# Kernel tuning notes

Measured on AMD Instinct MI355X. Metric: run time of the kernel, lower is better.

## Reference

```python
import jax, jax.numpy as jnp
import numpy as np

N = 100000
E = 640000
IN_DIM = 128
HID = 128
NUM_REL = 8


def _rgcn_layer(x, rel_w, root_w, bias, src, dst, edge_type, num_nodes):
    # PyG RGCNConv: out = x @ root + bias + sum_r mean_{edges of rel r into v}(x_src) @ W_r
    out = x @ root_w + bias
    x_src = x[src]  # [E, d_in]
    for r in range(NUM_REL):
        w = (edge_type == r).astype(x.dtype)  # [E]
        msg_sum = jax.ops.segment_sum(x_src * w[:, None], dst, num_segments=num_nodes)
        cnt = jax.ops.segment_sum(w, dst, num_segments=num_nodes)
        agg = msg_sum / jnp.maximum(cnt, 1.0)[:, None]  # mean aggregation per relation
        out = out + agg @ rel_w[r]
    return out


def setup_inputs() -> dict:
    key = jax.random.key(0)
    ks = jax.random.split(key, 10)
    x = jax.random.normal(ks[0], (N, IN_DIM), dtype=jnp.float32)
    edge_index = jax.random.randint(ks[1], (2, E), 0, N, dtype=jnp.int64)
    edge_type = jax.random.randint(ks[2], (E,), 0, NUM_REL, dtype=jnp.int64)
    s1 = 1.0 / np.sqrt(IN_DIM)
    s2 = 1.0 / np.sqrt(HID)
    rel_w1 = jax.random.uniform(ks[3], (NUM_REL, IN_DIM, HID), jnp.float32, -s1, s1)
    root_w1 = jax.random.uniform(ks[4], (IN_DIM, HID), jnp.float32, -s1, s1)
    b1 = jnp.zeros((HID,), jnp.float32)
    rel_w2 = jax.random.uniform(ks[5], (NUM_REL, HID, HID), jnp.float32, -s2, s2)
    root_w2 = jax.random.uniform(ks[6], (HID, HID), jnp.float32, -s2, s2)
    b2 = jnp.zeros((HID,), jnp.float32)
    return {"x": x, "edge_index": edge_index, "edge_type": edge_type,
            "rel_w1": rel_w1, "root_w1": root_w1, "b1": b1,
            "rel_w2": rel_w2, "root_w2": root_w2, "b2": b2}


def reference(x, edge_index, edge_type, rel_w1, root_w1, b1, rel_w2, root_w2, b2):
    src, dst = edge_index[0], edge_index[1]
    h = _rgcn_layer(x, rel_w1, root_w1, b1, src, dst, edge_type, N)
    h = jax.nn.relu(h)  # dropout p=0.0 -> identity
    h = _rgcn_layer(h, rel_w2, root_w2, b2, src, dst, edge_type, N)
    h = jax.nn.relu(h)
    return h
```

## Files before the change

kernel.cpp:

```cpp
#include <hip/hip_runtime.h>
#include <hip/hip_bf16.h>

#define NN 100000
#define EE 640000
#define DD 128
#define RR 8
#define K8 (NN * RR)
#define NSB2 196
#define GBMAX 11571

typedef __attribute__((ext_vector_type(8))) short short8;
typedef __attribute__((ext_vector_type(4))) float floatx4;
typedef __attribute__((ext_vector_type(4))) unsigned int uint4v;

__device__ __forceinline__ unsigned short f2bf(float f) {
  unsigned int u = __float_as_uint(f);
  u += 0x7FFFu + ((u >> 16) & 1u);
  return (unsigned short)(u >> 16);
}
__device__ __forceinline__ unsigned int pk2bf(float a, float b) {
  __hip_bfloat162 h = __float22bfloat162_rn(make_float2(a, b));
  unsigned int u;
  __builtin_memcpy(&u, &h, 4);
  return u;
}
__device__ __forceinline__ float bflo(unsigned int u) { return __uint_as_float(u << 16); }
__device__ __forceinline__ float bfhi(unsigned int u) { return __uint_as_float(u & 0xFFFF0000u); }

__global__ __launch_bounds__(256) void xb_prep(
    const float* __restrict__ x, unsigned int* __restrict__ xb)
{
  int g = blockIdx.x * 256 + threadIdx.x;
  int v = g >> 4, seg = g & 15;
  const float4* s4 = (const float4*)(x + (size_t)v * 128 + seg * 8);
  float4 a = s4[0], b = s4[1];
  uint4v o;
  o[0] = pk2bf(a.x, a.y); o[1] = pk2bf(a.z, a.w);
  o[2] = pk2bf(b.x, b.y); o[3] = pk2bf(b.z, b.w);
  *(uint4v*)(xb + (size_t)v * 64 + seg * 4) = o;
}

__global__ __launch_bounds__(256) void w_prep_all(
    const float* __restrict__ rel1, const float* __restrict__ root1,
    const float* __restrict__ rel2, const float* __restrict__ root2,
    unsigned short* __restrict__ wt)
{
  int id = blockIdx.x * 256 + threadIdx.x;
  int set = id >= 147456;
  int rem = id - set * 147456;
  int r = rem >> 14, n = (rem >> 7) & 127, k = rem & 127;
  const float* rel = set ? rel2 : rel1;
  const float* root = set ? root2 : root1;
  float v = (r < RR) ? rel[((size_t)r * DD + k) * DD + n] : root[(size_t)k * DD + n];
  wt[id] = f2bf(v);
}

__global__ __launch_bounds__(256) void count_all(
    const int* __restrict__ ei, const int* __restrict__ et,
    int* __restrict__ cntdr, unsigned char* __restrict__ used,
    int* __restrict__ erank)
{
  int e = blockIdx.x * 256 + threadIdx.x;
  int src = ei[e], dst = ei[EE + e], r = et[e];
  erank[e] = atomicAdd(&cntdr[dst * RR + r], 1);
  used[r * NN + src] = 1;
}

__global__ __launch_bounds__(256) void scan_a(
    const int4* __restrict__ c4, int n4, int* __restrict__ bsum)
{
  int t = threadIdx.x;
  int s = 0;
#pragma unroll
  for (int i = 0; i < 4; ++i) {
    int idx = blockIdx.x * 1024 + i * 256 + t;
    if (idx < n4) { int4 v = c4[idx]; s += v.x + v.y + v.z + v.w; }
  }
  __shared__ int wsum[4];
  for (int d = 32; d; d >>= 1) s += __shfl_xor(s, d, 64);
  if ((t & 63) == 0) wsum[t >> 6] = s;
  __syncthreads();
  if (t == 0) bsum[blockIdx.x] = wsum[0] + wsum[1] + wsum[2] + wsum[3];
}

__global__ __launch_bounds__(256) void scan_a_u8(
    const uint4v* __restrict__ c, int n16, int* __restrict__ bsum)
{
  int t = threadIdx.x;
  int idx = blockIdx.x * 256 + t;
  int s = 0;
  if (idx < n16) {
    uint4v v = c[idx];
#pragma unroll
    for (int w = 0; w < 4; ++w) {
      unsigned u = v[w];
      s += ((u & 0x000000FFu) ? 1 : 0) + ((u & 0x0000FF00u) ? 1 : 0)
         + ((u & 0x00FF0000u) ? 1 : 0) + ((u & 0xFF000000u) ? 1 : 0);
    }
  }
  __shared__ int wsum[4];
  for (int d = 32; d; d >>= 1) s += __shfl_xor(s, d, 64);
  if ((t & 63) == 0) wsum[t >> 6] = s;
  __syncthreads();
  if (t == 0) bsum[blockIdx.x] = wsum[0] + wsum[1] + wsum[2] + wsum[3];
}

__global__ void scan_b(const int* __restrict__ bsum, int nsb,
                       int* __restrict__ bbase, int* __restrict__ tot)
{
  int lane = threadIdx.x;
  int v[4]; int s = 0;
#pragma unroll
  for (int i = 0; i < 4; ++i) {
    int idx = lane * 4 + i;
    v[i] = (idx < nsb) ? bsum[idx] : 0; s += v[i];
  }
  int inc = s;
  for (int d = 1; d < 64; d <<= 1) {
    int o = __shfl_up(inc, d, 64);
    if (lane >= d) inc += o;
  }
  int running = inc - s;
#pragma unroll
  for (int i = 0; i < 4; ++i) {
    int idx = lane * 4 + i;
    if (idx < nsb) { bbase[idx] = running; running += v[i]; }
  }
  if (lane == 63 && tot != nullptr) tot[0] = inc;
}

__global__ __launch_bounds__(256) void scan_c(
    const int* __restrict__ cnt, const int* __restrict__ bbase, int n,
    int* __restrict__ out0)
{
  int t = threadIdx.x;
  int base = blockIdx.x * 4096 + t * 16;
  int v[16]; int s = 0;
#pragma unroll
  for (int i = 0; i < 16; ++i) {
    int idx = base + i;
    v[i] = (idx < n) ? cnt[idx] : 0;
    s += v[i];
  }
  int lane = t & 63, wid = t >> 6;
  int inc = s;
  for (int d = 1; d < 64; d <<= 1) {
    int o = __shfl_up(inc, d, 64);
    if (lane >= d) inc += o;
  }
  __shared__ int wsum[4];
  if (lane == 63) wsum[wid] = inc;
  __syncthreads();
  int wb = 0;
  for (int w = 0; w < wid; ++w) wb += wsum[w];
  int running = bbase[blockIdx.x] + wb + (inc - s);
#pragma unroll
  for (int i = 0; i < 16; ++i) {
    int idx = base + i;
    if (idx < n) { out0[idx] = running; running += v[i]; }
  }
  if (blockIdx.x == 0 && t == 0) out0[n] = EE;
}

__global__ __launch_bounds__(256) void scan_c_u8(
    const unsigned char* __restrict__ used, const int* __restrict__ bbase, int n,
    int* __restrict__ out0, int* __restrict__ ubp)
{
  int t = threadIdx.x;
  int base = blockIdx.x * 4096 + t * 16;
  int v[16]; int s = 0;
  if (base < n) {
    uint4v u = *(const uint4v*)(used + base);
    unsigned um[4]; *(uint4v*)um = u;
#pragma unroll
    for (int w = 0; w < 4; ++w)
#pragma unroll
      for (int b = 0; b < 4; ++b) {
        v[w * 4 + b] = ((um[w] >> (8 * b)) & 0xFFu) != 0;
        s += v[w * 4 + b];
      }
  } else {
#pragma unroll
    for (int i = 0; i < 16; ++i) v[i] = 0;
  }
  int lane = t & 63, wid = t >> 6;
  int inc = s;
  for (int d = 1; d < 64; d <<= 1) {
    int o = __shfl_up(inc, d, 64);
    if (lane >= d) inc += o;
  }
  __shared__ int wsum[4];
  if (lane == 63) wsum[wid] = inc;
  __syncthreads();
  int wb = 0;
  for (int w = 0; w < wid; ++w) wb += wsum[w];
  int running = bbase[blockIdx.x] + wb + (inc - s);
#pragma unroll
  for (int i = 0; i < 16; ++i) {
    int idx = base + i;
    if (idx < n) {
      if (idx % NN == 0) ubp[idx / NN] = running;
      out0[idx] = v[i] ? running : -1;
      running += v[i];
    }
  }
}

__global__ void pb_kernel(const int* __restrict__ ub, const int* __restrict__ tot,
                          int* __restrict__ pb)
{
  if (threadIdx.x == 0) {
    int base = 0;
    for (int r = 0; r < RR; ++r) {
      pb[r] = base;
      int hi = (r == RR - 1) ? tot[0] : ub[r + 1];
      int u = hi - ub[r];
      base += (u + 63) & ~63;
    }
    pb[8] = base;
    pb[9] = base + ((NN + 63) & ~63);
  }
}

__global__ __launch_bounds__(256) void fix_kernel(
    int* __restrict__ pidx, const int* __restrict__ ub,
    const int* __restrict__ pb, int* __restrict__ ysrc)
{
  int key = blockIdx.x * 256 + threadIdx.x;
  int g = pidx[key];
  if (g < 0) return;
  int r = key / NN, src = key - r * NN;
  int y = pb[r] + (g - ub[r]);
  pidx[key] = y;
  ysrc[y] = src;
}

__global__ __launch_bounds__(256) void place2(
    const int* __restrict__ ei, const int* __restrict__ et,
    const int* __restrict__ rowptr_dr, const int* __restrict__ pidx,
    const int* __restrict__ erank, int2* __restrict__ recs)
{
  int e = blockIdx.x * 256 + threadIdx.x;
  int src = ei[e], dst = ei[EE + e], r = et[e];
  int k = dst * RR + r;
  int b0 = rowptr_dr[k], b1 = rowptr_dr[k + 1];
  int slot = b0 + erank[e];
  float s = 1.0f / (float)max(b1 - b0, 1);
  int2 rec; rec.x = pidx[r * NN + src]; rec.y = __float_as_int(s);
  recs[slot] = rec;
}

__global__ __launch_bounds__(256, 3) void gemm_y(
    const unsigned int* __restrict__ Xb,
    const unsigned short* __restrict__ Wt,
    const int* __restrict__ ysrc,
    const int* __restrict__ pb,
    unsigned int* __restrict__ Ypk)
{
  const int yrow0 = blockIdx.x * 64;
  if (yrow0 >= pb[9]) return;
  int r = 8;
#pragma unroll
  for (int rr = 0; rr < 8; ++rr) if (yrow0 < pb[rr + 1]) { r = rr; break; }

  __shared__ unsigned short As[64 * 128];
  const int tid = threadIdx.x;
  const int wave = tid >> 6, lane = tid & 63;
  const int quad = lane >> 4, mr = lane & 15;
  const int pb8 = pb[8];

  {
    int row = tid >> 2, q = tid & 3;
    int yrow = yrow0 + row;
    int src;
    if (r < RR) src = ysrc[yrow];
    else { src = yrow - pb8; if (src >= NN) src = 0; }
    const uint4v* xs = (const uint4v*)(Xb + (size_t)src * 64 + q * 16);
#pragma unroll
    for (int c = 0; c < 4; ++c) {
      uint4v v = xs[c];
      int pos = (q * 32 + c * 8 + (row & 15) * 8) & 127;
      *(uint4v*)&As[row * 128 + pos] = v;
    }
  }
  const unsigned short* wr = Wt + (size_t)r * 16384 + (size_t)(wave * 32 + mr) * 128 + quad * 8;
  short8 b0[4], b1[4];
#pragma unroll
  for (int ks = 0; ks < 4; ++ks) {
    b0[ks] = *(const short8*)(wr + ks * 32);
    b1[ks] = *(const short8*)(wr + 16 * 128 + ks * 32);
  }
  __syncthreads();

  floatx4 acc[4][2];
#pragma unroll
  for (int mi = 0; mi < 4; ++mi) {
    acc[mi][0] = (floatx4){0.f, 0.f, 0.f, 0.f};
    acc[mi][1] = (floatx4){0.f, 0.f, 0.f, 0.f};
  }
#pragma unroll
  for (int ks = 0; ks < 4; ++ks) {
    short8 a[4];
#pragma unroll
    for (int mi = 0; mi < 4; ++mi)
      a[mi] = *(const short8*)&As[(mi * 16 + mr) * 128 +
                                  ((ks * 32 + quad * 8 + mr * 8) & 127)];
#pragma unroll
    for (int mi = 0; mi < 4; ++mi) {
      acc[mi][0] = __builtin_amdgcn_mfma_f32_16x16x32_bf16(a[mi], b0[ks], acc[mi][0], 0, 0, 0);
      acc[mi][1] = __builtin_amdgcn_mfma_f32_16x16x32_bf16(a[mi], b1[ks], acc[mi][1], 0, 0, 0);
    }
  }
#pragma unroll
  for (int mi = 0; mi < 4; ++mi)
#pragma unroll
    for (int rg = 0; rg < 4; ++rg)
      Ypk[(size_t)(yrow0 + mi * 16 + quad * 4 + rg) * 64 + wave * 16 + mr] =
          pk2bf(acc[mi][0][rg], acc[mi][1][rg]);
}

__global__ __launch_bounds__(256) void aggregate(
    const unsigned int* __restrict__ Ypk,
    const int* __restrict__ rowptr,
    const int2* __restrict__ recs,
    const int* __restrict__ pb,
    const float* __restrict__ bias,
    void* __restrict__ outp, int out_bf16)
{
  int gid = blockIdx.x * 256 + threadIdx.x;
  int v = gid >> 4;
  int o = gid & 7;
  int h = (gid >> 3) & 1;
  int c0 = 32 * (o >> 1) + 8 * (o & 1);
  int pb8 = pb[8];

  float lo[8], hi[8];
  if (h == 0) {
    const uint4v* rp = (const uint4v*)(Ypk + (size_t)(pb8 + v) * 64 + o * 8);
    uint4v u0 = rp[0], u1 = rp[1];
    unsigned um[8];
    *(uint4v*)&um[0] = u0; *(uint4v*)&um[4] = u1;
#pragma unroll
    for (int j = 0; j < 8; ++j) {
      lo[j] = bias[c0 + j] + bflo(um[j]);
      hi[j] = bias[c0 + 16 + j] + bfhi(um[j]);
    }
  } else {
#pragma unroll
    for (int j = 0; j < 8; ++j) { lo[j] = 0.f; hi[j] = 0.f; }
  }

  int beg = rowptr[v * RR], end = rowptr[v * RR + RR];
  int e = beg + h;
  if (e < end) {
    int2 rec = recs[e];
    const uint4v* yp = (const uint4v*)(Ypk + (size_t)rec.x * 64 + o * 8);
    uint4v c0v = yp[0], c1v = yp[1];
    for (; e < end; e += 2) {
      int2 nrec = rec;
      uint4v n0 = c0v, n1 = c1v;
      if (e + 2 < end) {
        nrec = recs[e + 2];
        const uint4v* np = (const uint4v*)(Ypk + (size_t)nrec.x * 64 + o * 8);
        n0 = np[0]; n1 = np[1];
      }
      float s = __int_as_float(rec.y);
      unsigned um[8];
      *(uint4v*)&um[0] = c0v; *(uint4v*)&um[4] = c1v;
#pragma unroll
      for (int j = 0; j < 8; ++j) {
        lo[j] = fmaf(s, bflo(um[j]), lo[j]);
        hi[j] = fmaf(s, bfhi(um[j]), hi[j]);
      }
      rec = nrec; c0v = n0; c1v = n1;
    }
  }

#pragma unroll
  for (int j = 0; j < 8; ++j) {
    lo[j] += __shfl_xor(lo[j], 8, 64);
    hi[j] += __shfl_xor(hi[j], 8, 64);
  }
  if (h) return;

#pragma unroll
  for (int j = 0; j < 8; ++j) {
    lo[j] = fmaxf(lo[j], 0.f);
    hi[j] = fmaxf(hi[j], 0.f);
  }

  if (out_bf16) {
    unsigned int* hh = (unsigned int*)outp;
    uint4v wl, wh;
#pragma unroll
    for (int t = 0; t < 4; ++t) {
      wl[t] = pk2bf(lo[2 * t], lo[2 * t + 1]);
      wh[t] = pk2bf(hi[2 * t], hi[2 * t + 1]);
    }
    *(uint4v*)&hh[(size_t)v * 64 + c0 / 2] = wl;
    *(uint4v*)&hh[(size_t)v * 64 + c0 / 2 + 8] = wh;
  } else {
    float* out = (float*)outp;
    float4* dl = (float4*)(out + (size_t)v * 128 + c0);
    float4* dh = (float4*)(out + (size_t)v * 128 + c0 + 16);
    dl[0] = make_float4(lo[0], lo[1], lo[2], lo[3]);
    dl[1] = make_float4(lo[4], lo[5], lo[6], lo[7]);
    dh[0] = make_float4(hi[0], hi[1], hi[2], hi[3]);
    dh[1] = make_float4(hi[4], hi[5], hi[6], hi[7]);
  }
}

extern "C" void kernel_launch(void* const* d_in, const int* in_sizes, int n_in,
                              void* d_out, int out_size, void* d_ws, size_t ws_size,
                              hipStream_t stream) {
  const float* x       = (const float*)d_in[0];
  const int*   ei      = (const int*)d_in[1];
  const int*   et      = (const int*)d_in[2];
  const float* rel_w1  = (const float*)d_in[3];
  const float* root_w1 = (const float*)d_in[4];
  const float* b1      = (const float*)d_in[5];
  const float* rel_w2  = (const float*)d_in[6];
  const float* root_w2 = (const float*)d_in[7];
  const float* b2      = (const float*)d_in[8];

  char* ws = (char*)d_ws;
  size_t off = 0;
  auto alloc = [&](size_t bytes) { char* p = ws + off; off = (off + bytes + 255) & ~(size_t)255; return p; };
  unsigned int*   Ypk   = (unsigned int*)alloc((size_t)(EE + NN + 1024) * 64 * 4);
  unsigned int*   Xb    = (unsigned int*)alloc((size_t)NN * 64 * 4);
  unsigned int*   h1    = (unsigned int*)alloc((size_t)NN * 64 * 4);
  unsigned short* Wt    = (unsigned short*)alloc((size_t)2 * 9 * DD * DD * 2);
  int*            cntdr = (int*)alloc((size_t)K8 * 4);
  unsigned char*  used  = (unsigned char*)alloc((size_t)K8);
  int*            ysrc  = (int*)alloc((size_t)(EE + 1024) * 4);
  char*           zend  = ws + off;
  int*            rowptr_dr = (int*)alloc((size_t)(K8 + 1) * 4);
  int*            erank = (int*)alloc((size_t)EE * 4);
  int*            pidx  = (int*)alloc((size_t)K8 * 4);
  int2*           recs  = (int2*)alloc((size_t)EE * 8);
  int*            bsumA = (int*)alloc((size_t)NSB2 * 4);
  int*            bbaseA= (int*)alloc((size_t)NSB2 * 4);
  int*            bsumB = (int*)alloc((size_t)NSB2 * 4);
  int*            bbaseB= (int*)alloc((size_t)NSB2 * 4);
  int*            ub    = (int*)alloc(64);
  int*            pb    = (int*)alloc(64);
  int*            Ptot  = (int*)alloc(64);

  hipMemsetAsync(cntdr, 0, (size_t)(zend - (char*)cntdr), stream);

  xb_prep<<<(NN * 16) / 256, 256, 0, stream>>>(x, Xb);
  w_prep_all<<<(2 * 9 * DD * DD) / 256, 256, 0, stream>>>(rel_w1, root_w1, rel_w2, root_w2, Wt);
  count_all<<<EE / 256, 256, 0, stream>>>(ei, et, cntdr, used, erank);

  scan_a<<<NSB2, 256, 0, stream>>>((const int4*)cntdr, K8 / 4, bsumA);
  scan_b<<<1, 64, 0, stream>>>(bsumA, NSB2, bbaseA, nullptr);
  scan_c<<<NSB2, 256, 0, stream>>>(cntdr, bbaseA, K8, rowptr_dr);

  scan_a_u8<<<NSB2, 256, 0, stream>>>((const uint4v*)used, K8 / 16, bsumB);
  scan_b<<<1, 64, 0, stream>>>(bsumB, NSB2, bbaseB, Ptot);
  scan_c_u8<<<NSB2, 256, 0, stream>>>(used, bbaseB, K8, pidx, ub);
  pb_kernel<<<1, 64, 0, stream>>>(ub, Ptot, pb);
  fix_kernel<<<K8 / 256, 256, 0, stream>>>(pidx, ub, pb, ysrc);

  place2<<<EE / 256, 256, 0, stream>>>(ei, et, rowptr_dr, pidx, erank, recs);

  const int AB = (NN * 16) / 256;

  gemm_y<<<GBMAX, 256, 0, stream>>>(Xb, Wt, ysrc, pb, Ypk);
  aggregate<<<AB, 256, 0, stream>>>(Ypk, rowptr_dr, recs, pb, b1, h1, 1);
  gemm_y<<<GBMAX, 256, 0, stream>>>(h1, Wt + (size_t)9 * DD * DD, ysrc, pb, Ypk);
  aggregate<<<AB, 256, 0, stream>>>(Ypk, rowptr_dr, recs, pb, b2, d_out, 0);
}
```

Before: 377.9 us.

## Fuse prep and scan kernels, add XCD-aware block remap in gemm_y

Merges xb_prep, w_prep_all and count_all into one prep_all launch. Merges the two three-stage scans (edge counts and used flags) into scan_ab, scan_b2 and scan_c_both, cutting nine launches down to four. gemm_y now remaps blockIdx so that consecutive row tiles land on the same XCD, aiming for better L2 reuse of the weight and gathered rows. The intent is to cut launch overhead and improve cache locality. The cost is that each fused kernel is more complex.

```diff
diff --git a/kernel.cpp b/kernel.cpp
--- a/kernel.cpp
+++ b/kernel.cpp
@@ -8,6 +8,9 @@
 #define K8 (NN * RR)
 #define NSB2 196
 #define GBMAX 11571
+#define CNTB (EE / 256)
+#define XBB ((NN * 16) / 256)
+#define WPB ((2 * 9 * DD * DD) / 256)
 
 typedef __attribute__((ext_vector_type(8))) short short8;
 typedef __attribute__((ext_vector_type(4))) float floatx4;
@@ -27,93 +30,88 @@
 __device__ __forceinline__ float bflo(unsigned int u) { return __uint_as_float(u << 16); }
 __device__ __forceinline__ float bfhi(unsigned int u) { return __uint_as_float(u & 0xFFFF0000u); }
 
-__global__ __launch_bounds__(256) void xb_prep(
-    const float* __restrict__ x, unsigned int* __restrict__ xb)
-{
-  int g = blockIdx.x * 256 + threadIdx.x;
-  int v = g >> 4, seg = g & 15;
-  const float4* s4 = (const float4*)(x + (size_t)v * 128 + seg * 8);
-  float4 a = s4[0], b = s4[1];
-  uint4v o;
-  o[0] = pk2bf(a.x, a.y); o[1] = pk2bf(a.z, a.w);
-  o[2] = pk2bf(b.x, b.y); o[3] = pk2bf(b.z, b.w);
-  *(uint4v*)(xb + (size_t)v * 64 + seg * 4) = o;
-}
-
-__global__ __launch_bounds__(256) void w_prep_all(
+__global__ __launch_bounds__(256) void prep_all(
+    const float* __restrict__ x, unsigned int* __restrict__ xb,
     const float* __restrict__ rel1, const float* __restrict__ root1,
     const float* __restrict__ rel2, const float* __restrict__ root2,
-    unsigned short* __restrict__ wt)
-{
-  int id = blockIdx.x * 256 + threadIdx.x;
-  int set = id >= 147456;
-  int rem = id - set * 147456;
-  int r = rem >> 14, n = (rem >> 7) & 127, k = rem & 127;
-  const float* rel = set ? rel2 : rel1;
-  const float* root = set ? root2 : root1;
-  float v = (r < RR) ? rel[((size_t)r * DD + k) * DD + n] : root[(size_t)k * DD + n];
-  wt[id] = f2bf(v);
-}
-
-__global__ __launch_bounds__(256) void count_all(
+    unsigned short* __restrict__ wt,
     const int* __restrict__ ei, const int* __restrict__ et,
     int* __restrict__ cntdr, unsigned char* __restrict__ used,
     int* __restrict__ erank)
 {
-  int e = blockIdx.x * 256 + threadIdx.x;
-  int src = ei[e], dst = ei[EE + e], r = et[e];
-  erank[e] = atomicAdd(&cntdr[dst * RR + r], 1);
-  used[r * NN + src] = 1;
-}
-
-__global__ __launch_bounds__(256) void scan_a(
-    const int4* __restrict__ c4, int n4, int* __restrict__ bsum)
+  int b = blockIdx.x, t = threadIdx.x;
+  if (b < CNTB) {
+    int e = b * 256 + t;
+    int src = ei[e], dst = ei[EE + e], r = et[e];
+    erank[e] = atomicAdd(&cntdr[dst * RR + r], 1);
+    used[r * NN + src] = 1;
+  } else if (b < CNTB + XBB) {
+    int g = (b - CNTB) * 256 + t;
+    int v = g >> 4, seg = g & 15;
+    const float4* s4 = (const float4*)(x + (size_t)v * 128 + seg * 8);
+    float4 a = s4[0], bb = s4[1];
+    uint4v o;
+    o[0] = pk2bf(a.x, a.y); o[1] = pk2bf(a.z, a.w);
+    o[2] = pk2bf(bb.x, bb.y); o[3] = pk2bf(bb.z, bb.w);
+    *(uint4v*)(xb + (size_t)v * 64 + seg * 4) = o;
+  } else {
+    int id = (b - CNTB - XBB) * 256 + t;
+    int set = id >= 147456;
+    int rem = id - set * 147456;
+    int r = rem >> 14, n = (rem >> 7) & 127, k = rem & 127;
+    const float* rel = set ? rel2 : rel1;
+    const float* root = set ? root2 : root1;
+    float v = (r < RR) ? rel[((size_t)r * DD + k) * DD + n] : root[(size_t)k * DD + n];
+    wt[id] = f2bf(v);
+  }
+}
+
+__global__ __launch_bounds__(256) void scan_ab(
+    const int4* __restrict__ c4, const uint4v* __restrict__ u16,
+    int n4, int n16, int* __restrict__ bsumA, int* __restrict__ bsumB)
 {
   int t = threadIdx.x;
-  int s = 0;
+  int sA = 0;
 #pragma unroll
   for (int i = 0; i < 4; ++i) {
     int idx = blockIdx.x * 1024 + i * 256 + t;
-    if (idx < n4) { int4 v = c4[idx]; s += v.x + v.y + v.z + v.w; }
-  }
-  __shared__ int wsum[4];
-  for (int d = 32; d; d >>= 1) s += __shfl_xor(s, d, 64);
-  if ((t & 63) == 0) wsum[t >> 6] = s;
+    if (idx < n4) { int4 v = c4[idx]; sA += v.x + v.y + v.z + v.w; }
+  }
+  int sB = 0;
+  {
+    int idx = blockIdx.x * 256 + t;
+    if (idx < n16) {
+      uint4v v = u16[idx];
+#pragma unroll
+      for (int w = 0; w < 4; ++w) {
+        unsigned u = v[w];
+        sB += ((u & 0x000000FFu) ? 1 : 0) + ((u & 0x0000FF00u) ? 1 : 0)
+            + ((u & 0x00FF0000u) ? 1 : 0) + ((u & 0xFF000000u) ? 1 : 0);
+      }
+    }
+  }
+  for (int d = 32; d; d >>= 1) { sA += __shfl_xor(sA, d, 64); sB += __shfl_xor(sB, d, 64); }
+  __shared__ int wsA[4], wsB[4];
+  if ((t & 63) == 0) { wsA[t >> 6] = sA; wsB[t >> 6] = sB; }
   __syncthreads();
-  if (t == 0) bsum[blockIdx.x] = wsum[0] + wsum[1] + wsum[2] + wsum[3];
-}
-
-__global__ __launch_bounds__(256) void scan_a_u8(
-    const uint4v* __restrict__ c, int n16, int* __restrict__ bsum)
-{
-  int t = threadIdx.x;
-  int idx = blockIdx.x * 256 + t;
-  int s = 0;
-  if (idx < n16) {
-    uint4v v = c[idx];
-#pragma unroll
-    for (int w = 0; w < 4; ++w) {
-      unsigned u = v[w];
-      s += ((u & 0x000000FFu) ? 1 : 0) + ((u & 0x0000FF00u) ? 1 : 0)
-         + ((u & 0x00FF0000u) ? 1 : 0) + ((u & 0xFF000000u) ? 1 : 0);
-    }
-  }
-  __shared__ int wsum[4];
-  for (int d = 32; d; d >>= 1) s += __shfl_xor(s, d, 64);
-  if ((t & 63) == 0) wsum[t >> 6] = s;
-  __syncthreads();
-  if (t == 0) bsum[blockIdx.x] = wsum[0] + wsum[1] + wsum[2] + wsum[3];
-}
-
-__global__ void scan_b(const int* __restrict__ bsum, int nsb,
-                       int* __restrict__ bbase, int* __restrict__ tot)
-{
-  int lane = threadIdx.x;
+  if (t == 0) {
+    bsumA[blockIdx.x] = wsA[0] + wsA[1] + wsA[2] + wsA[3];
+    bsumB[blockIdx.x] = wsB[0] + wsB[1] + wsB[2] + wsB[3];
+  }
+}
+
+__global__ void scan_b2(const int* __restrict__ bsumA, const int* __restrict__ bsumB,
+                        int nsb, int* __restrict__ bbaseA, int* __restrict__ bbaseB,
+                        int* __restrict__ tot)
+{
+  int wid = threadIdx.x >> 6, lane = threadIdx.x & 63;
+  const int* bs = wid ? bsumB : bsumA;
+  int* bb = wid ? bbaseB : bbaseA;
   int v[4]; int s = 0;
 #pragma unroll
   for (int i = 0; i < 4; ++i) {
     int idx = lane * 4 + i;
-    v[i] = (idx < nsb) ? bsum[idx] : 0; s += v[i];
+    v[i] = (idx < nsb) ? bs[idx] : 0; s += v[i];
   }
   int inc = s;
   for (int d = 1; d < 64; d <<= 1) {
@@ -124,84 +122,82 @@
 #pragma unroll
   for (int i = 0; i < 4; ++i) {
     int idx = lane * 4 + i;
-    if (idx < nsb) { bbase[idx] = running; running += v[i]; }
-  }
-  if (lane == 63 && tot != nullptr) tot[0] = inc;
-}
-
-__global__ __launch_bounds__(256) void scan_c(
-    const int* __restrict__ cnt, const int* __restrict__ bbase, int n,
-    int* __restrict__ out0)
+    if (idx < nsb) { bb[idx] = running; running += v[i]; }
+  }
+  if (wid == 1 && lane == 63) tot[0] = inc;
+}
+
+__global__ __launch_bounds__(256) void scan_c_both(
+    const int* __restrict__ cnt, const unsigned char* __restrict__ used,
+    const int* __restrict__ bbaseA, const int* __restrict__ bbaseB, int n,
+    int* __restrict__ rowptr, int* __restrict__ pidx, int* __restrict__ ubp)
 {
   int t = threadIdx.x;
   int base = blockIdx.x * 4096 + t * 16;
-  int v[16]; int s = 0;
-#pragma unroll
-  for (int i = 0; i < 16; ++i) {
-    int idx = base + i;
-    v[i] = (idx < n) ? cnt[idx] : 0;
-    s += v[i];
-  }
   int lane = t & 63, wid = t >> 6;
-  int inc = s;
-  for (int d = 1; d < 64; d <<= 1) {
-    int o = __shfl_up(inc, d, 64);
-    if (lane >= d) inc += o;
-  }
   __shared__ int wsum[4];
-  if (lane == 63) wsum[wid] = inc;
+
+  {
+    int v[16]; int s = 0;
+#pragma unroll
+    for (int i = 0; i < 16; ++i) {
+      int idx = base + i;
+      v[i] = (idx < n) ? cnt[idx] : 0;
+      s += v[i];
+    }
+    int inc = s;
+    for (int d = 1; d < 64; d <<= 1) {
+      int o = __shfl_up(inc, d, 64);
+      if (lane >= d) inc += o;
+    }
+    if (lane == 63) wsum[wid] = inc;
+    __syncthreads();
+    int wb = 0;
+    for (int w = 0; w < wid; ++w) wb += wsum[w];
+    int running = bbaseA[blockIdx.x] + wb + (inc - s);
+#pragma unroll
+    for (int i = 0; i < 16; ++i) {
+      int idx = base + i;
+      if (idx < n) { rowptr[idx] = running; running += v[i]; }
+    }
+    if (blockIdx.x == 0 && t == 0) rowptr[n] = EE;
+  }
   __syncthreads();
-  int wb = 0;
-  for (int w = 0; w < wid; ++w) wb += wsum[w];
-  int running = bbase[blockIdx.x] + wb + (inc - s);
-#pragma unroll
-  for (int i = 0; i < 16; ++i) {
-    int idx = base + i;
-    if (idx < n) { out0[idx] = running; running += v[i]; }
-  }
-  if (blockIdx.x == 0 && t == 0) out0[n] = EE;
-}
-
-__global__ __launch_bounds__(256) void scan_c_u8(
-    const unsigned char* __restrict__ used, const int* __restrict__ bbase, int n,
-    int* __restrict__ out0, int* __restrict__ ubp)
-{
-  int t = threadIdx.x;
-  int base = blockIdx.x * 4096 + t * 16;
-  int v[16]; int s = 0;
-  if (base < n) {
-    uint4v u = *(const uint4v*)(used + base);
-    unsigned um[4]; *(uint4v*)um = u;
-#pragma unroll
-    for (int w = 0; w < 4; ++w)
-#pragma unroll
-      for (int b = 0; b < 4; ++b) {
-        v[w * 4 + b] = ((um[w] >> (8 * b)) & 0xFFu) != 0;
-        s += v[w * 4 + b];
+
+  {
+    int v[16]; int s = 0;
+    if (base < n) {
+      uint4v u = *(const uint4v*)(used + base);
+      unsigned um[4]; *(uint4v*)um = u;
+#pragma unroll
+      for (int w = 0; w < 4; ++w)
+#pragma unroll
+        for (int b = 0; b < 4; ++b) {
+          v[w * 4 + b] = ((um[w] >> (8 * b)) & 0xFFu) != 0;
+          s += v[w * 4 + b];
+        }
+    } else {
+#pragma unroll
+      for (int i = 0; i < 16; ++i) v[i] = 0;
+    }
+    int inc = s;
+    for (int d = 1; d < 64; d <<= 1) {
+      int o = __shfl_up(inc, d, 64);
+      if (lane >= d) inc += o;
+    }
+    if (lane == 63) wsum[wid] = inc;
+    __syncthreads();
+    int wb = 0;
+    for (int w = 0; w < wid; ++w) wb += wsum[w];
+    int running = bbaseB[blockIdx.x] + wb + (inc - s);
+#pragma unroll
+    for (int i = 0; i < 16; ++i) {
+      int idx = base + i;
+      if (idx < n) {
+        if (idx % NN == 0) ubp[idx / NN] = running;
+        pidx[idx] = v[i] ? running : -1;
+        running += v[i];
       }
-  } else {
-#pragma unroll
-    for (int i = 0; i < 16; ++i) v[i] = 0;
-  }
-  int lane = t & 63, wid = t >> 6;
-  int inc = s;
-  for (int d = 1; d < 64; d <<= 1) {
-    int o = __shfl_up(inc, d, 64);
-    if (lane >= d) inc += o;
-  }
-  __shared__ int wsum[4];
-  if (lane == 63) wsum[wid] = inc;
-  __syncthreads();
-  int wb = 0;
-  for (int w = 0; w < wid; ++w) wb += wsum[w];
-  int running = bbase[blockIdx.x] + wb + (inc - s);
-#pragma unroll
-  for (int i = 0; i < 16; ++i) {
-    int idx = base + i;
-    if (idx < n) {
-      if (idx % NN == 0) ubp[idx / NN] = running;
-      out0[idx] = v[i] ? running : -1;
-      running += v[i];
     }
   }
 }
@@ -257,7 +253,13 @@
     const int* __restrict__ pb,
     unsigned int* __restrict__ Ypk)
 {
-  const int yrow0 = blockIdx.x * 64;
+  const int nwg = gridDim.x;
+  const int q = nwg >> 3, rmd = nwg & 7;
+  int bid = blockIdx.x;
+  int xcd = bid & 7, idx = bid >> 3;
+  int wgid = (xcd < rmd ? xcd * (q + 1) : rmd * (q + 1) + (xcd - rmd) * q) + idx;
+
+  const int yrow0 = wgid * 64;
   if (yrow0 >= pb[9]) return;
   int r = 8;
 #pragma unroll
@@ -270,16 +272,16 @@
   const int pb8 = pb[8];
 
   {
-    int row = tid >> 2, q = tid & 3;
+    int row = tid >> 2, qq = tid & 3;
     int yrow = yrow0 + row;
     int src;
     if (r < RR) src = ysrc[yrow];
     else { src = yrow - pb8; if (src >= NN) src = 0; }
-    const uint4v* xs = (const uint4v*)(Xb + (size_t)src * 64 + q * 16);
+    const uint4v* xs = (const uint4v*)(Xb + (size_t)src * 64 + qq * 16);
 #pragma unroll
     for (int c = 0; c < 4; ++c) {
       uint4v v = xs[c];
-      int pos = (q * 32 + c * 8 + (row & 15) * 8) & 127;
+      int pos = (qq * 32 + c * 8 + (row & 15) * 8) & 127;
       *(uint4v*)&As[row * 128 + pos] = v;
     }
   }
@@ -448,20 +450,17 @@
 
   hipMemsetAsync(cntdr, 0, (size_t)(zend - (char*)cntdr), stream);
 
-  xb_prep<<<(NN * 16) / 256, 256, 0, stream>>>(x, Xb);
-  w_prep_all<<<(2 * 9 * DD * DD) / 256, 256, 0, stream>>>(rel_w1, root_w1, rel_w2, root_w2, Wt);
-  count_all<<<EE / 256, 256, 0, stream>>>(ei, et, cntdr, used, erank);
-
-  scan_a<<<NSB2, 256, 0, stream>>>((const int4*)cntdr, K8 / 4, bsumA);
-  scan_b<<<1, 64, 0, stream>>>(bsumA, NSB2, bbaseA, nullptr);
-  scan_c<<<NSB2, 256, 0, stream>>>(cntdr, bbaseA, K8, rowptr_dr);
-
-  scan_a_u8<<<NSB2, 256, 0, stream>>>((const uint4v*)used, K8 / 16, bsumB);
-  scan_b<<<1, 64, 0, stream>>>(bsumB, NSB2, bbaseB, Ptot);
-  scan_c_u8<<<NSB2, 256, 0, stream>>>(used, bbaseB, K8, pidx, ub);
+  prep_all<<<CNTB + XBB + WPB, 256, 0, stream>>>(
+      x, Xb, rel_w1, root_w1, rel_w2, root_w2, Wt, ei, et, cntdr, used, erank);
+
+  scan_ab<<<NSB2, 256, 0, stream>>>((const int4*)cntdr, (const uint4v*)used,
+                                    K8 / 4, K8 / 16, bsumA, bsumB);
+  scan_b2<<<1, 128, 0, stream>>>(bsumA, bsumB, NSB2, bbaseA, bbaseB, Ptot);
+  scan_c_both<<<NSB2, 256, 0, stream>>>(cntdr, used, bbaseA, bbaseB, K8,
+                                        rowptr_dr, pidx, ub);
+
   pb_kernel<<<1, 64, 0, stream>>>(ub, Ptot, pb);
   fix_kernel<<<K8 / 256, 256, 0, stream>>>(pidx, ub, pb, ysrc);
-
   place2<<<EE / 256, 256, 0, stream>>>(ei, et, rowptr_dr, pidx, erank, recs);
 
   const int AB = (NN * 16) / 256;
```

Result: slower. 394.3 us (+4.3%).
